# Optimization experiments

Measured on AMD Instinct MI355X. Metric: run time of the kernel, lower is better.

Reference implementation:

```python
import jax, jax.numpy as jnp
import numpy as np
import math

B, S, H, D = 1, 2048, 12, 128
DIM = H * D
BLKQ, BLKK = 128, 64
TOPK = 0.2
EPS = 1e-6
NEG = -1e30


def setup_inputs() -> dict:
    key = jax.random.key(0)
    ks = jax.random.split(key, 8)
    hidden_states = jax.random.normal(ks[0], (B, S, DIM), jnp.float32)
    # interleaved RoPE tables: even slots hold cos, odd slots hold sin phase copies
    pos = np.arange(S, dtype=np.float64)[:, None]
    inv = 1.0 / (10000.0 ** (np.arange(0, D, 2, dtype=np.float64) / D))
    ang = pos * inv[None, :]                       # [S, D/2]
    freqs_cos = jnp.asarray(np.repeat(np.cos(ang), 2, axis=-1), jnp.float32).reshape(1, S, 1, D)
    freqs_sin = jnp.asarray(np.repeat(np.sin(ang), 2, axis=-1), jnp.float32).reshape(1, S, 1, D)
    sc = 1.0 / math.sqrt(DIM)
    Wq = jax.random.normal(ks[1], (DIM, DIM), jnp.float32) * sc
    Wk = jax.random.normal(ks[2], (DIM, DIM), jnp.float32) * sc
    Wv = jax.random.normal(ks[3], (DIM, DIM), jnp.float32) * sc
    Wo = jax.random.normal(ks[4], (DIM, DIM), jnp.float32) * sc
    bq = jax.random.normal(ks[5], (DIM,), jnp.float32) * 0.01
    bk = jax.random.normal(ks[6], (DIM,), jnp.float32) * 0.01
    bv = jax.random.normal(ks[7], (DIM,), jnp.float32) * 0.01
    bo = jnp.zeros((DIM,), jnp.float32)
    gq = jnp.ones((DIM,), jnp.float32)
    gk = jnp.ones((DIM,), jnp.float32)
    return dict(hidden_states=hidden_states, freqs_cos=freqs_cos, freqs_sin=freqs_sin,
                Wq=Wq, bq=bq, Wk=Wk, bk=bk, Wv=Wv, bv=bv, Wo=Wo, bo=bo, gq=gq, gk=gk)


def _rmsnorm(x, g):
    return x * jax.lax.rsqrt(jnp.mean(x * x, axis=-1, keepdims=True) + EPS) * g


def _rope(x, fc, fs):
    # x: [B,S,H,D]; interleaved even/odd rotation as in _apply_rotary_emb
    x1 = x[..., 0::2]
    x2 = x[..., 1::2]
    cos = fc[..., 0::2]
    sin = fs[..., 1::2]
    even = x1 * cos - x2 * sin
    odd = x1 * sin + x2 * cos
    return jnp.stack([even, odd], axis=-1).reshape(x.shape)


def _sla(q, k, v):
    # q,k,v: [B,H,S,D]. Top-k block-sparse exact attention + linear attention
    # (softmax feature map) on the unselected blocks, jointly normalized.
    nqb, nkb = S // BLKQ, S // BLKK
    ksel = max(1, int(math.ceil(TOPK * nkb)))
    qb = q.reshape(B, H, nqb, BLKQ, D).mean(axis=3)
    kb = k.reshape(B, H, nkb, BLKK, D).mean(axis=3)
    blk_scores = jnp.einsum('bhqd,bhkd->bhqk', qb, kb)
    _, idx = jax.lax.top_k(blk_scores, ksel)                  # [B,H,nqb,ksel]
    bmask = (jax.nn.one_hot(idx, nkb, dtype=jnp.float32).sum(axis=-2) > 0)
    mask = jnp.repeat(jnp.repeat(bmask, BLKQ, axis=2), BLKK, axis=3)  # [B,H,S,S]

    scale = 1.0 / math.sqrt(D)
    s = jnp.einsum('bhqd,bhkd->bhqk', q, k) * scale
    m = jnp.max(jnp.where(mask, s, NEG), axis=-1, keepdims=True)
    p = jnp.where(mask, jnp.exp(s - m), 0.0)
    num_s = jnp.einsum('bhqk,bhkd->bhqd', p, v)
    den_s = p.sum(axis=-1, keepdims=True)

    lq = jax.nn.softmax(q, axis=-1)
    lk = jax.nn.softmax(k, axis=-1)
    L = jnp.where(mask, 0.0, jnp.einsum('bhqd,bhkd->bhqk', lq, lk))
    num_l = jnp.einsum('bhqk,bhkd->bhqd', L, v)
    den_l = L.sum(axis=-1, keepdims=True)

    w = jnp.exp(-m)  # bring linear part onto the max-shifted exp scale
    return (num_s + w * num_l) / (den_s + w * den_l)


def reference(hidden_states, freqs_cos, freqs_sin, Wq, bq, Wk, bk, Wv, bv, Wo, bo, gq, gk):
    q = _rmsnorm(hidden_states @ Wq + bq, gq).reshape(B, S, H, D)
    k = _rmsnorm(hidden_states @ Wk + bk, gk).reshape(B, S, H, D)
    v = (hidden_states @ Wv + bv).reshape(B, S, H, D)
    q = _rope(q, freqs_cos, freqs_sin)
    k = _rope(k, freqs_cos, freqs_sin)
    q, k, v = (t.transpose(0, 2, 1, 3) for t in (q, k, v))  # [B,H,S,D]
    o = _sla(q, k, v)
    o = o.transpose(0, 2, 1, 3).reshape(B, S, DIM)
    return o @ Wo + bo
```

## Files before the change

### kernel.cpp

```cpp
#include <hip/hip_runtime.h>
#include <hip/hip_bf16.h>

#define SQ   2048
#define DIMM 1536
#define QS   4608
#define NH   12
#define DH   128
#define NQB  16
#define NKB  32
#define KSEL 7

typedef unsigned short u16;
typedef __bf16 bf16x8 __attribute__((ext_vector_type(8)));
typedef _Float16 f16x8 __attribute__((ext_vector_type(8)));
typedef short  s16x8  __attribute__((ext_vector_type(8)));
typedef float  f32x4  __attribute__((ext_vector_type(4)));

__device__ __forceinline__ float bf2f(u16 u) {
  unsigned int x = ((unsigned int)u) << 16;
  return __builtin_bit_cast(float, x);
}
__device__ __forceinline__ u16 f2bf(float f) {
  unsigned int x = __builtin_bit_cast(unsigned int, f);
  x += 0x7fffu + ((x >> 16) & 1u);
  return (u16)(x >> 16);
}

typedef __attribute__((address_space(3))) void lds_vt;
typedef const __attribute__((address_space(1))) void g_vt;
__device__ __forceinline__ void dma16(const void* g, void* l) {
  __builtin_amdgcn_global_load_lds((g_vt*)g, (lds_vt*)l, 16, 0, 0);
}

__global__ __launch_bounds__(256) void prep_hs(const float* __restrict__ hs,
                                               u16* __restrict__ hh,
                                               u16* __restrict__ hl) {
  size_t i = ((size_t)blockIdx.x * 256 + threadIdx.x) * 8;
  f32x4 a = *(const f32x4*)&hs[i];
  f32x4 b = *(const f32x4*)&hs[i + 4];
  s16x8 h, l;
  #pragma unroll
  for (int j = 0; j < 4; j++) {
    u16 hj = f2bf(a[j]); h[j] = (short)hj; l[j] = (short)f2bf(a[j] - bf2f(hj));
    u16 hk = f2bf(b[j]); h[4 + j] = (short)hk; l[4 + j] = (short)f2bf(b[j] - bf2f(hk));
  }
  *(s16x8*)&hh[i] = h;
  *(s16x8*)&hl[i] = l;
}

__global__ __launch_bounds__(256) void prep_w(const float* __restrict__ W0,
                                              const float* __restrict__ W1,
                                              const float* __restrict__ W2,
                                              const float* __restrict__ W3,
                                              u16* __restrict__ WTh,
                                              u16* __restrict__ WTl) {
  __shared__ float tile[64][65];
  int wi = blockIdx.z;
  const float* W = (wi == 0) ? W0 : (wi == 1) ? W1 : (wi == 2) ? W2 : W3;
  int x = threadIdx.x & 63, y = threadIdx.x >> 6;
  int k0 = blockIdx.y * 64, n0 = blockIdx.x * 64;
  #pragma unroll
  for (int i = 0; i < 16; i++) {
    int k = y + i * 4;
    tile[k][x] = W[(size_t)(k0 + k) * DIMM + n0 + x];
  }
  __syncthreads();
  size_t obase = (size_t)wi * DIMM * DIMM;
  #pragma unroll
  for (int i = 0; i < 16; i++) {
    int n = y + i * 4;
    float v = tile[x][n];
    size_t oi = obase + (size_t)(n0 + n) * DIMM + k0 + x;
    if (wi == 3) {
      WTh[oi] = __builtin_bit_cast(u16, (_Float16)v);
    } else {
      u16 h = f2bf(v);
      WTh[oi] = h;
      WTl[oi] = f2bf(v - bf2f(h));
    }
  }
}

__global__ __launch_bounds__(256) void gemm3_k(const u16* __restrict__ Ahp,
                                               const u16* __restrict__ Alp,
                                               const u16* __restrict__ WTh,
                                               const u16* __restrict__ WTl,
                                               const float* __restrict__ bq,
                                               const float* __restrict__ bk,
                                               const float* __restrict__ bv,
                                               float* __restrict__ C) {
  __shared__ u16 As[2][128][64];
  __shared__ u16 Bs[2][128][64];
  const int tid = threadIdx.x;
  const int w = tid >> 6, lane = tid & 63, quad = lane >> 4, l16 = lane & 15;
  const int wr = w >> 1, wc = w & 1;
  const int m_base = blockIdx.y * 128;
  const int nt = blockIdx.x;
  const int wi = nt / 12;
  const int n_in = (nt % 12) * 128;
  const u16* Bh0 = WTh + ((size_t)wi * DIMM + n_in) * DIMM;
  const u16* Bl0 = WTl + ((size_t)wi * DIMM + n_in) * DIMM;
  const float* bias = (wi == 0) ? bq : (wi == 1) ? bk : bv;
  const bool split = (wi != 2);

  const int srow = lane >> 3;
  const int skc = (((lane & 7) ^ srow) * 8);
  const int rx = (l16 & 7);

  f32x4 zero4 = {0.f, 0.f, 0.f, 0.f};
  f32x4 acc[4][4];
  #pragma unroll
  for (int i = 0; i < 4; i++)
    #pragma unroll
    for (int j = 0; j < 4; j++) acc[i][j] = zero4;

  for (int k0 = 0; k0 < DIMM; k0 += 64) {
    #pragma unroll
    for (int c = 0; c < 4; c++) {
      int r0 = w * 32 + c * 8;
      int row = r0 + srow;
      dma16(&Ahp[(size_t)(m_base + row) * DIMM + k0 + skc], &As[0][r0][0]);
      dma16(&Bh0[(size_t)row * DIMM + k0 + skc], &Bs[0][r0][0]);
      if (split) {
        dma16(&Alp[(size_t)(m_base + row) * DIMM + k0 + skc], &As[1][r0][0]);
        dma16(&Bl0[(size_t)row * DIMM + k0 + skc], &Bs[1][r0][0]);
      }
    }
    __syncthreads();
    #pragma unroll
    for (int kk = 0; kk < 2; kk++) {
      const int coff = ((kk * 4 + quad) ^ rx) * 8;
      bf16x8 afh[4], afl[4], bfh[4], bfl[4];
      #pragma unroll
      for (int i = 0; i < 4; i++)
        afh[i] = __builtin_bit_cast(bf16x8,
                 *(const s16x8*)&As[0][wr * 64 + i * 16 + l16][coff]);
      #pragma unroll
      for (int j = 0; j < 4; j++)
        bfh[j] = __builtin_bit_cast(bf16x8,
                 *(const s16x8*)&Bs[0][wc * 64 + j * 16 + l16][coff]);
      if (split) {
        #pragma unroll
        for (int i = 0; i < 4; i++)
          afl[i] = __builtin_bit_cast(bf16x8,
                   *(const s16x8*)&As[1][wr * 64 + i * 16 + l16][coff]);
        #pragma unroll
        for (int j = 0; j < 4; j++)
          bfl[j] = __builtin_bit_cast(bf16x8,
                   *(const s16x8*)&Bs[1][wc * 64 + j * 16 + l16][coff]);
      }
      #pragma unroll
      for (int i = 0; i < 4; i++)
        #pragma unroll
        for (int j = 0; j < 4; j++) {
          acc[i][j] = __builtin_amdgcn_mfma_f32_16x16x32_bf16(afh[i], bfh[j], acc[i][j], 0, 0, 0);
          if (split) {
            acc[i][j] = __builtin_amdgcn_mfma_f32_16x16x32_bf16(afh[i], bfl[j], acc[i][j], 0, 0, 0);
            acc[i][j] = __builtin_amdgcn_mfma_f32_16x16x32_bf16(afl[i], bfh[j], acc[i][j], 0, 0, 0);
          }
        }
    }
    __syncthreads();
  }
  #pragma unroll
  for (int i = 0; i < 4; i++)
    #pragma unroll
    for (int j = 0; j < 4; j++) {
      int tc = wc * 64 + j * 16 + l16;
      float bv2 = bias[n_in + tc];
      #pragma unroll
      for (int rg = 0; rg < 4; rg++) {
        int r = m_base + wr * 64 + i * 16 + quad * 4 + rg;
        C[(size_t)r * QS + nt * 128 + tc] = acc[i][j][rg] + bv2;
      }
    }
}

__global__ __launch_bounds__(256) void gemm_o(const u16* __restrict__ Ap,
                                              const u16* __restrict__ Bp,
                                              const float* __restrict__ bias,
                                              float* __restrict__ C) {
  __shared__ u16 As[64][64];
  __shared__ u16 Bs[128][64];
  const int tid = threadIdx.x;
  const int w = tid >> 6, lane = tid & 63, quad = lane >> 4, l16 = lane & 15;
  const int wr = w >> 1, wc = w & 1;
  const int m_base = blockIdx.y * 64, n_base = blockIdx.x * 128;
  const int srow = lane >> 3;
  const int skc = (((lane & 7) ^ srow) * 8);
  const int rx = (l16 & 7);

  f32x4 zero4 = {0.f, 0.f, 0.f, 0.f};
  f32x4 acc[2][4];
  #pragma unroll
  for (int i = 0; i < 2; i++)
    #pragma unroll
    for (int j = 0; j < 4; j++) acc[i][j] = zero4;

  for (int k0 = 0; k0 < DIMM; k0 += 64) {
    #pragma unroll
    for (int c = 0; c < 2; c++) {
      int r0 = w * 16 + c * 8;
      int row = r0 + srow;
      dma16(&Ap[(size_t)(m_base + row) * DIMM + k0 + skc], &As[r0][0]);
    }
    #pragma unroll
    for (int c = 0; c < 4; c++) {
      int r0 = w * 32 + c * 8;
      int row = r0 + srow;
      dma16(&Bp[(size_t)(n_base + row) * DIMM + k0 + skc], &Bs[r0][0]);
    }
    __syncthreads();
    #pragma unroll
    for (int kk = 0; kk < 2; kk++) {
      const int coff = ((kk * 4 + quad) ^ rx) * 8;
      f16x8 af[2], bf[4];
      #pragma unroll
      for (int i = 0; i < 2; i++)
        af[i] = __builtin_bit_cast(f16x8,
                *(const s16x8*)&As[wr * 32 + i * 16 + l16][coff]);
      #pragma unroll
      for (int j = 0; j < 4; j++)
        bf[j] = __builtin_bit_cast(f16x8,
                *(const s16x8*)&Bs[wc * 64 + j * 16 + l16][coff]);
      #pragma unroll
      for (int i = 0; i < 2; i++)
        #pragma unroll
        for (int j = 0; j < 4; j++)
          acc[i][j] = __builtin_amdgcn_mfma_f32_16x16x32_f16(af[i], bf[j], acc[i][j], 0, 0, 0);
    }
    __syncthreads();
  }
  #pragma unroll
  for (int i = 0; i < 2; i++)
    #pragma unroll
    for (int j = 0; j < 4; j++) {
      int c = n_base + wc * 64 + j * 16 + l16;
      float bv2 = bias[c];
      #pragma unroll
      for (int rg = 0; rg < 4; rg++) {
        int r = m_base + wr * 32 + i * 16 + quad * 4 + rg;
        C[(size_t)r * DIMM + c] = acc[i][j][rg] + bv2;
      }
    }
}

__global__ __launch_bounds__(256) void norm_rope_k(float* __restrict__ qkv,
                                                   const float* __restrict__ gq,
                                                   const float* __restrict__ gk,
                                                   const float* __restrict__ fc,
                                                   const float* __restrict__ fs) {
  int s = blockIdx.x;
  float* row = qkv + (size_t)s * QS + (blockIdx.y == 0 ? 0 : DIMM);
  const float* g = (blockIdx.y == 0) ? gq : gk;
  int t = threadIdx.x;
  float ss = 0.f;
  #pragma unroll
  for (int i = 0; i < 6; i++) {
    float v = row[t + i * 256];
    ss += v * v;
  }
  #pragma unroll
  for (int m = 1; m < 64; m <<= 1) ss += __shfl_xor(ss, m, 64);
  __shared__ float wsum[4];
  if ((t & 63) == 0) wsum[t >> 6] = ss;
  __syncthreads();
  float tot = wsum[0] + wsum[1] + wsum[2] + wsum[3];
  float sc = rsqrtf(tot / 1536.0f + 1e-6f);
  #pragma unroll
  for (int i = 0; i < 3; i++) {
    int p = t + i * 256;
    int h = p >> 6, ip = p & 63;
    int base = h * 128 + 2 * ip;
    float x1 = row[base] * sc * g[base];
    float x2 = row[base + 1] * sc * g[base + 1];
    float c = fc[(size_t)s * 128 + 2 * ip];
    float sn = fs[(size_t)s * 128 + 2 * ip + 1];
    row[base]     = x1 * c - x2 * sn;
    row[base + 1] = x1 * sn + x2 * c;
  }
}

__global__ __launch_bounds__(256) void prep_qk(const float* __restrict__ qkv,
                                               u16* __restrict__ qbf,
                                               u16* __restrict__ kbf) {
  int s0 = blockIdx.x * 128, h = blockIdx.y, z = blockIdx.z;
  int off = z * DIMM;
  u16* out = (z ? kbf : qbf) + ((size_t)h * SQ + s0) * 128;
  int tid = threadIdx.x;
  #pragma unroll
  for (int i = 0; i < 8; i++) {
    int idx = i * 256 + tid;
    int r = idx >> 4, c = idx & 15;
    int g = (c & 8) | ((c ^ (r & 7)) & 7);
    const float* src = qkv + (size_t)(s0 + r) * QS + off + h * DH + g * 8;
    f32x4 a = *(const f32x4*)src;
    f32x4 b = *(const f32x4*)(src + 4);
    s16x8 o;
    #pragma unroll
    for (int e = 0; e < 4; e++) { o[e] = (short)f2bf(a[e]); o[4 + e] = (short)f2bf(b[e]); }
    *(s16x8*)&out[r * 128 + c * 8] = o;
  }
}

__global__ __launch_bounds__(256) void prep_vT(const float* __restrict__ vf,
                                               u16* __restrict__ vbfT) {
  __shared__ float vt[64][132];
  int b = blockIdx.x, h = blockIdx.y, tid = threadIdx.x;
  #pragma unroll
  for (int i = 0; i < 8; i++) {
    int idx = i * 256 + tid; int key = idx >> 5, d4 = (idx & 31) * 4;
    *(f32x4*)&vt[key][d4] = *(const f32x4*)&vf[(size_t)(b * 64 + key) * QS + h * DH + d4];
  }
  __syncthreads();
  u16* out = vbfT + ((size_t)(h * NKB + b)) * 128 * 64;
  #pragma unroll
  for (int i = 0; i < 4; i++) {
    int idx = i * 256 + tid;
    int d = idx >> 3, c = idx & 7;
    int g = c ^ (d & 7);
    s16x8 o;
    #pragma unroll
    for (int e = 0; e < 8; e++) o[e] = (short)f2bf(vt[g * 8 + e][d]);
    *(s16x8*)&out[d * 64 + c * 8] = o;
  }
}

__global__ __launch_bounds__(128) void means_k(const float* __restrict__ qf,
                                               const float* __restrict__ kf,
                                               float* __restrict__ qb,
                                               float* __restrict__ kb) {
  int h = blockIdx.y, t = threadIdx.x;
  if (blockIdx.x < NQB) {
    int qi = blockIdx.x;
    float a = 0.f;
    for (int r = 0; r < 128; r++) a += qf[(size_t)(qi * 128 + r) * QS + h * DH + t];
    qb[(h * NQB + qi) * DH + t] = a * (1.0f / 128.0f);
  } else {
    int ki = blockIdx.x - NQB;
    float a = 0.f;
    for (int r = 0; r < 64; r++) a += kf[(size_t)(ki * 64 + r) * QS + h * DH + t];
    kb[(h * NKB + ki) * DH + t] = a * (1.0f / 64.0f);
  }
}

__global__ __launch_bounds__(64) void topk_k(const float* __restrict__ qb,
                                             const float* __restrict__ kb,
                                             int* __restrict__ sel) {
  int h = blockIdx.y, qi = blockIdx.x, t = threadIdx.x;
  __shared__ float scs[NKB];
  if (t < NKB) {
    float a = 0.f;
    for (int d = 0; d < DH; d++)
      a += qb[(h * NQB + qi) * DH + d] * kb[(h * NKB + t) * DH + d];
    scs[t] = a;
  }
  __syncthreads();
  if (t == 0) {
    unsigned int used = 0;
    for (int it = 0; it < KSEL; it++) {
      float best = -3.4e38f; int bi = 0;
      for (int j = 0; j < NKB; j++)
        if (!((used >> j) & 1) && scs[j] > best) { best = scs[j]; bi = j; }
      used |= 1u << bi;
      sel[(h * NQB + qi) * 8 + it] = bi;
    }
  }
}

__global__ __launch_bounds__(256) void kv_k(const float* __restrict__ kf,
                                            const float* __restrict__ vf,
                                            float* __restrict__ KV,
                                            float* __restrict__ slk) {
  int h = blockIdx.y, kb = blockIdx.x, t = threadIdx.x;
  __shared__ float lkt[64][128];
  __shared__ float vt[64][128];
  #pragma unroll
  for (int i = 0; i < 8; i++) {
    int idx = i * 256 + t; int r = idx >> 5, d4 = (idx & 31) * 4;
    *(f32x4*)&vt[r][d4] = *(const f32x4*)&vf[(size_t)(kb * 64 + r) * QS + h * DH + d4];
  }
  if (t < 64) {
    const float* kr = kf + (size_t)(kb * 64 + t) * QS + h * DH;
    float m = -3.4e38f;
    for (int d = 0; d < 128; d++) m = fmaxf(m, kr[d]);
    float sum = 0.f;
    for (int d = 0; d < 128; d++) { float e = __expf(kr[d] - m); lkt[t][d] = e; sum += e; }
    float inv = 1.0f / sum;
    for (int d = 0; d < 128; d++) lkt[t][d] *= inv;
  }
  __syncthreads();
  int d1 = t >> 1, hf = t & 1;
  float acc[64];
  #pragma unroll
  for (int i = 0; i < 64; i++) acc[i] = 0.f;
  for (int j = 0; j < 64; j++) {
    float lv = lkt[j][d1];
    #pragma unroll
    for (int dd = 0; dd < 64; dd++) acc[dd] += lv * vt[j][hf * 64 + dd];
  }
  float* out = KV + ((size_t)(h * NKB + kb) * DH + d1) * DH + hf * 64;
  #pragma unroll
  for (int dd = 0; dd < 64; dd++) out[dd] = acc[dd];
  if (t < 128) {
    float a = 0.f;
    for (int j = 0; j < 64; j++) a += lkt[j][t];
    slk[(h * NKB + kb) * DH + t] = a;
  }
}

__global__ __launch_bounds__(256) void kvtot_k(const float* __restrict__ KV,
                                               const float* __restrict__ slk,
                                               float* __restrict__ KVtot,
                                               float* __restrict__ sltot) {
  int h = blockIdx.y; int e = blockIdx.x * 256 + threadIdx.x;
  float a = 0.f;
  for (int b = 0; b < NKB; b++) a += KV[(size_t)(h * NKB + b) * 16384 + e];
  KVtot[(size_t)h * 16384 + e] = a;
  if (blockIdx.x == 0 && threadIdx.x < 128) {
    float s2 = 0.f;
    for (int b = 0; b < NKB; b++) s2 += slk[(h * NKB + b) * DH + threadIdx.x];
    sltot[h * DH + threadIdx.x] = s2;
  }
}

__global__ __launch_bounds__(256) void attn_k(const u16* __restrict__ qbf,
                                              const u16* __restrict__ kbf,
                                              const u16* __restrict__ vbfT,
                                              const int* __restrict__ sel,
                                              const float* __restrict__ KV,
                                              const float* __restrict__ slk,
                                              const float* __restrict__ KVtot,
                                              const float* __restrict__ sltot,
                                              u16* __restrict__ of16) {
  __shared__ u16 qt[128 * 128];
  __shared__ u16 kt[64 * 128];
  __shared__ u16 vtT[128 * 64];
  __shared__ u16 ptb[128][72];
  __shared__ u16 MT[128][136];
  __shared__ float mrow[128], lrow[128], dent[128], slsh[128];
  __shared__ int selsh[KSEL];

  int h = blockIdx.y, qi = blockIdx.x, tid = threadIdx.x;
  int w = tid >> 6, lane = tid & 63, quad = lane >> 4, l16 = lane & 15;

  {
    const u16* qsrc = qbf + ((size_t)h * SQ + qi * 128) * 128;
    #pragma unroll
    for (int c = 0; c < 8; c++)
      dma16(qsrc + (w * 32 + c * 4) * 128 + lane * 8, &qt[(w * 32 + c * 4) * 128]);
  }
  if (tid < KSEL) selsh[tid] = sel[(h * NQB + qi) * 8 + tid];
  __syncthreads();

  float m_run[2][4], l_run[2][4];
  f32x4 zero4 = {0.f, 0.f, 0.f, 0.f};
  f32x4 oacc[2][8];
  #pragma unroll
  for (int mt = 0; mt < 2; mt++) {
    #pragma unroll
    for (int rg = 0; rg < 4; rg++) { m_run[mt][rg] = -3.0e38f; l_run[mt][rg] = 0.f; }
    #pragma unroll
    for (int nt = 0; nt < 8; nt++) oacc[mt][nt] = zero4;
  }

  for (int bi = 0; bi < KSEL; bi++) {
    int b = selsh[bi];
    {
      const u16* ksrc = kbf + ((size_t)h * SQ + b * 64) * 128;
      #pragma unroll
      for (int c = 0; c < 4; c++)
        dma16(ksrc + (w * 16 + c * 4) * 128 + lane * 8, &kt[(w * 16 + c * 4) * 128]);
      const u16* vsrc = vbfT + ((size_t)(h * NKB + b)) * 128 * 64;
      #pragma unroll
      for (int c = 0; c < 4; c++)
        dma16(vsrc + (w * 32 + c * 8) * 64 + lane * 8, &vtT[(w * 32 + c * 8) * 64]);
    }
    __syncthreads();

    f32x4 sacc[2][4];
    #pragma unroll
    for (int mt = 0; mt < 2; mt++)
      #pragma unroll
      for (int nt = 0; nt < 4; nt++) sacc[mt][nt] = zero4;
    #pragma unroll
    for (int kk = 0; kk < 4; kk++) {
      const int kkq = kk * 4 + quad;
      const int qoff = ((kkq & 8) | ((kkq ^ (l16 & 7)) & 7)) * 8;
      bf16x8 af[2], bfr[4];
      af[0] = __builtin_bit_cast(bf16x8, *(const s16x8*)&qt[(w * 32 + l16) * 128 + qoff]);
      af[1] = __builtin_bit_cast(bf16x8, *(const s16x8*)&qt[(w * 32 + 16 + l16) * 128 + qoff]);
      #pragma unroll
      for (int nt = 0; nt < 4; nt++)
        bfr[nt] = __builtin_bit_cast(bf16x8, *(const s16x8*)&kt[(nt * 16 + l16) * 128 + qoff]);
      #pragma unroll
      for (int mt = 0; mt < 2; mt++)
        #pragma unroll
        for (int nt = 0; nt < 4; nt++)
          sacc[mt][nt] = __builtin_amdgcn_mfma_f32_16x16x32_bf16(af[mt], bfr[nt], sacc[mt][nt], 0, 0, 0);
    }
    const float SCALE = 0.08838834764831845f;
    #pragma unroll
    for (int mt = 0; mt < 2; mt++)
      #pragma unroll
      for (int nt = 0; nt < 4; nt++) sacc[mt][nt] *= SCALE;

    #pragma unroll
    for (int mt = 0; mt < 2; mt++) {
      #pragma unroll
      for (int rg = 0; rg < 4; rg++) {
        float bmax = fmaxf(fmaxf(sacc[mt][0][rg], sacc[mt][1][rg]),
                           fmaxf(sacc[mt][2][rg], sacc[mt][3][rg]));
        bmax = fmaxf(bmax, __shfl_xor(bmax, 1, 64));
        bmax = fmaxf(bmax, __shfl_xor(bmax, 2, 64));
        bmax = fmaxf(bmax, __shfl_xor(bmax, 4, 64));
        bmax = fmaxf(bmax, __shfl_xor(bmax, 8, 64));
        float mold = m_run[mt][rg];
        float mnew = fmaxf(mold, bmax);
        float alpha = __expf(mold - mnew);
        float rs = 0.f;
        #pragma unroll
        for (int nt = 0; nt < 4; nt++) {
          float p = __expf(sacc[mt][nt][rg] - mnew);
          sacc[mt][nt][rg] = p; rs += p;
        }
        rs += __shfl_xor(rs, 1, 64);
        rs += __shfl_xor(rs, 2, 64);
        rs += __shfl_xor(rs, 4, 64);
        rs += __shfl_xor(rs, 8, 64);
        m_run[mt][rg] = mnew;
        l_run[mt][rg] = l_run[mt][rg] * alpha + rs;
        #pragma unroll
        for (int nt = 0; nt < 8; nt++) oacc[mt][nt][rg] *= alpha;
        int r = w * 32 + mt * 16 + quad * 4 + rg;
        #pragma unroll
        for (int nt = 0; nt < 4; nt++) ptb[r][nt * 16 + l16] = f2bf(sacc[mt][nt][rg]);
      }
    }
    __syncthreads();
    #pragma unroll
    for (int kk = 0; kk < 2; kk++) {
      bf16x8 pa[2];
      pa[0] = __builtin_bit_cast(bf16x8, *(const s16x8*)&ptb[w * 32 + l16][kk * 32 + quad * 8]);
      pa[1] = __builtin_bit_cast(bf16x8, *(const s16x8*)&ptb[w * 32 + 16 + l16][kk * 32 + quad * 8]);
      #pragma unroll
      for (int nt = 0; nt < 8; nt++) {
        const int voff = ((kk * 4 + quad) ^ (l16 & 7)) * 8;
        bf16x8 vb = __builtin_bit_cast(bf16x8, *(const s16x8*)&vtT[(nt * 16 + l16) * 64 + voff]);
        oacc[0][nt] = __builtin_amdgcn_mfma_f32_16x16x32_bf16(pa[0], vb, oacc[0][nt], 0, 0, 0);
        oacc[1][nt] = __builtin_amdgcn_mfma_f32_16x16x32_bf16(pa[1], vb, oacc[1][nt], 0, 0, 0);
      }
    }
    __syncthreads();
  }

  if (l16 == 0) {
    #pragma unroll
    for (int mt = 0; mt < 2; mt++)
      #pragma unroll
      for (int rg = 0; rg < 4; rg++) {
        int r = w * 32 + mt * 16 + quad * 4 + rg;
        mrow[r] = m_run[mt][rg];
        lrow[r] = l_run[mt][rg];
      }
  }
  if (tid < 128) {
    float a = sltot[h * DH + tid];
    #pragma unroll
    for (int i = 0; i < KSEL; i++) a -= slk[(h * NKB + selsh[i]) * DH + tid];
    slsh[tid] = a;
  }
  for (int i = 0; i < 16; i++) {
    int idx = i * 256 + tid;
    int e4 = idx * 4;
    int d1 = e4 >> 7, d2 = e4 & 127;
    f32x4 a = *(const f32x4*)&KVtot[(size_t)h * 16384 + e4];
    #pragma unroll
    for (int k2 = 0; k2 < KSEL; k2++) {
      f32x4 s4 = *(const f32x4*)&KV[(size_t)(h * NKB + selsh[k2]) * 16384 + e4];
      a -= s4;
    }
    #pragma unroll
    for (int j = 0; j < 4; j++) MT[d2 + j][d1] = f2bf(a[j]);
  }
  __syncthreads();

  {
    int r = tid >> 1, hf2 = tid & 1;
    float w_r = __expf(-mrow[r]);
    float mx = -3.4e38f;
    #pragma unroll
    for (int g = 0; g < 8; g++) {
      int gc = hf2 * 8 + g;
      int c = (gc & 8) | ((gc ^ (r & 7)) & 7);
      #pragma unroll
      for (int e = 0; e < 8; e++) mx = fmaxf(mx, bf2f(qt[r * 128 + c * 8 + e]));
    }
    mx = fmaxf(mx, __shfl_xor(mx, 1, 64));
    float sum = 0.f;
    #pragma unroll
    for (int g = 0; g < 8; g++) {
      int gc = hf2 * 8 + g;
      int c = (gc & 8) | ((gc ^ (r & 7)) & 7);
      #pragma unroll
      for (int e = 0; e < 8; e++) sum += __expf(bf2f(qt[r * 128 + c * 8 + e]) - mx);
    }
    sum += __shfl_xor(sum, 1, 64);
    float sc2 = w_r / sum;
    float dl = 0.f;
    #pragma unroll
    for (int g = 0; g < 8; g++) {
      int gc = hf2 * 8 + g;
      int c = (gc & 8) | ((gc ^ (r & 7)) & 7);
      #pragma unroll
      for (int e = 0; e < 8; e++) {
        float lq = __expf(bf2f(qt[r * 128 + c * 8 + e]) - mx) * sc2;
        dl += lq * slsh[gc * 8 + e];
        qt[r * 128 + c * 8 + e] = f2bf(lq);
      }
    }
    dl += __shfl_xor(dl, 1, 64);
    if (hf2 == 0) dent[r] = lrow[r] + dl;
  }
  __syncthreads();

  #pragma unroll
  for (int kk = 0; kk < 4; kk++) {
    const int kkq = kk * 4 + quad;
    const int qoff = ((kkq & 8) | ((kkq ^ (l16 & 7)) & 7)) * 8;
    bf16x8 af0 = __builtin_bit_cast(bf16x8, *(const s16x8*)&qt[(w * 32 + l16) * 128 + qoff]);
    bf16x8 af1 = __builtin_bit_cast(bf16x8, *(const s16x8*)&qt[(w * 32 + 16 + l16) * 128 + qoff]);
    #pragma unroll
    for (int nt = 0; nt < 8; nt++) {
      bf16x8 mb = __builtin_bit_cast(bf16x8, *(const s16x8*)&MT[nt * 16 + l16][kk * 32 + quad * 8]);
      oacc[0][nt] = __builtin_amdgcn_mfma_f32_16x16x32_bf16(af0, mb, oacc[0][nt], 0, 0, 0);
      oacc[1][nt] = __builtin_amdgcn_mfma_f32_16x16x32_bf16(af1, mb, oacc[1][nt], 0, 0, 0);
    }
  }

  #pragma unroll
  for (int mt = 0; mt < 2; mt++)
    #pragma unroll
    for (int rg = 0; rg < 4; rg++) {
      int r = w * 32 + mt * 16 + quad * 4 + rg;
      float inv = 1.0f / dent[r];
      #pragma unroll
      for (int nt = 0; nt < 8; nt++) {
        int c = nt * 16 + l16;
        float v = oacc[mt][nt][rg] * inv;
        size_t oi = (size_t)(qi * 128 + r) * DIMM + h * DH + c;
        of16[oi] = __builtin_bit_cast(u16, (_Float16)v);
      }
    }
}

extern "C" void kernel_launch(void* const* d_in, const int* in_sizes, int n_in,
                              void* d_out, int out_size, void* d_ws, size_t ws_size,
                              hipStream_t stream) {
  const float* hs = (const float*)d_in[0];
  const float* fc = (const float*)d_in[1];
  const float* fs = (const float*)d_in[2];
  const float* Wq = (const float*)d_in[3];
  const float* bq = (const float*)d_in[4];
  const float* Wk = (const float*)d_in[5];
  const float* bk = (const float*)d_in[6];
  const float* Wv = (const float*)d_in[7];
  const float* bv = (const float*)d_in[8];
  const float* Wo = (const float*)d_in[9];
  const float* bo = (const float*)d_in[10];
  const float* gq = (const float*)d_in[11];
  const float* gk = (const float*)d_in[12];

  char* p = (char*)d_ws;
  auto alloc = [&](size_t bytes) {
    char* r = p; p += (bytes + 255) & ~(size_t)255; return r;
  };
  u16* WTh = (u16*)alloc((size_t)4 * DIMM * DIMM * 2);
  u16* WTl = (u16*)alloc((size_t)4 * DIMM * DIMM * 2);
  u16* hsh = (u16*)alloc((size_t)SQ * DIMM * 2);
  u16* hsl = (u16*)alloc((size_t)SQ * DIMM * 2);
  float* qkv = (float*)alloc((size_t)SQ * QS * 4);
  u16* qbf = (u16*)alloc((size_t)NH * SQ * DH * 2);
  u16* kbf = (u16*)alloc((size_t)NH * SQ * DH * 2);
  u16* vbfT = (u16*)alloc((size_t)NH * NKB * DH * 64 * 2);
  float* qb = (float*)alloc((size_t)NH * NQB * DH * 4);
  float* kb = (float*)alloc((size_t)NH * NKB * DH * 4);
  int* sel = (int*)alloc((size_t)NH * NQB * 8 * 4);
  float* KV = (float*)alloc((size_t)NH * NKB * DH * DH * 4);
  float* slk = (float*)alloc((size_t)NH * NKB * DH * 4);
  float* KVtot = (float*)alloc((size_t)NH * DH * DH * 4);
  float* sltot = (float*)alloc((size_t)NH * DH * 4);

  float* qf = qkv;
  float* kf = qkv + DIMM;
  float* vf = qkv + 2 * DIMM;

  prep_hs<<<SQ * DIMM / (256 * 8), 256, 0, stream>>>(hs, hsh, hsl);
  prep_w<<<dim3(24, 24, 4), 256, 0, stream>>>(Wq, Wk, Wv, Wo, WTh, WTl);

  gemm3_k<<<dim3(36, 16), 256, 0, stream>>>(hsh, hsl, WTh, WTl, bq, bk, bv, qkv);

  norm_rope_k<<<dim3(SQ, 2), 256, 0, stream>>>(qkv, gq, gk, fc, fs);
  means_k<<<dim3(NQB + NKB, NH), 128, 0, stream>>>(qf, kf, qb, kb);
  topk_k<<<dim3(NQB, NH), 64, 0, stream>>>(qb, kb, sel);
  kv_k<<<dim3(NKB, NH), 256, 0, stream>>>(kf, vf, KV, slk);
  kvtot_k<<<dim3(64, NH), 256, 0, stream>>>(KV, slk, KVtot, sltot);
  prep_qk<<<dim3(16, NH, 2), 256, 0, stream>>>(qkv, qbf, kbf);
  prep_vT<<<dim3(NKB, NH), 256, 0, stream>>>(vf, vbfT);

  u16* of16 = hsh;
  attn_k<<<dim3(NQB, NH), 256, 0, stream>>>(qbf, kbf, vbfT, sel, KV, slk, KVtot, sltot, of16);

  const u16* WTo = WTh + (size_t)3 * DIMM * DIMM;
  gemm_o<<<dim3(12, 32), 256, 0, stream>>>(of16, WTo, bo, (float*)d_out);
}
```

Baseline: 369.0 us.

## Fuse bf16 Q/K packing into norm-rope, split attention blocks, vectorize kv_k

Several independent changes. The norm/RoPE kernel now also writes the swizzled bf16 Q/K copies directly, so the separate prep_qk pass and its reread of qkv go away. The attention kernel handles 64 query rows per block instead of 128, doubling the grid to 384 blocks for better CU occupancy. It also aliases shared-memory buffers to cut LDS use and raises wave priority around the MFMA sections. kv_k now computes the key softmax with all 256 threads and vectorized loads, pads its LDS rows, and accumulates with float4 vectors; in exchange the attention block's K/V loads are spread over twice as many blocks.

```diff
diff --git a/kernel.cpp b/kernel.cpp
--- a/kernel.cpp
+++ b/kernel.cpp
@@ -249,10 +249,13 @@
                                                    const float* __restrict__ gq,
                                                    const float* __restrict__ gk,
                                                    const float* __restrict__ fc,
-                                                   const float* __restrict__ fs) {
+                                                   const float* __restrict__ fs,
+                                                   u16* __restrict__ qbf,
+                                                   u16* __restrict__ kbf) {
   int s = blockIdx.x;
   float* row = qkv + (size_t)s * QS + (blockIdx.y == 0 ? 0 : DIMM);
   const float* g = (blockIdx.y == 0) ? gq : gk;
+  u16* obase = (blockIdx.y == 0) ? qbf : kbf;
   int t = threadIdx.x;
   float ss = 0.f;
   #pragma unroll
@@ -276,30 +279,15 @@
     float x2 = row[base + 1] * sc * g[base + 1];
     float c = fc[(size_t)s * 128 + 2 * ip];
     float sn = fs[(size_t)s * 128 + 2 * ip + 1];
-    row[base]     = x1 * c - x2 * sn;
-    row[base + 1] = x1 * sn + x2 * c;
-  }
-}
-
-__global__ __launch_bounds__(256) void prep_qk(const float* __restrict__ qkv,
-                                               u16* __restrict__ qbf,
-                                               u16* __restrict__ kbf) {
-  int s0 = blockIdx.x * 128, h = blockIdx.y, z = blockIdx.z;
-  int off = z * DIMM;
-  u16* out = (z ? kbf : qbf) + ((size_t)h * SQ + s0) * 128;
-  int tid = threadIdx.x;
-  #pragma unroll
-  for (int i = 0; i < 8; i++) {
-    int idx = i * 256 + tid;
-    int r = idx >> 4, c = idx & 15;
-    int g = (c & 8) | ((c ^ (r & 7)) & 7);
-    const float* src = qkv + (size_t)(s0 + r) * QS + off + h * DH + g * 8;
-    f32x4 a = *(const f32x4*)src;
-    f32x4 b = *(const f32x4*)(src + 4);
-    s16x8 o;
-    #pragma unroll
-    for (int e = 0; e < 4; e++) { o[e] = (short)f2bf(a[e]); o[4 + e] = (short)f2bf(b[e]); }
-    *(s16x8*)&out[r * 128 + c * 8] = o;
+    float ev = x1 * c - x2 * sn;
+    float od = x1 * sn + x2 * c;
+    row[base]     = ev;
+    row[base + 1] = od;
+    int gsk = ip >> 2, e = (2 * ip) & 7;
+    int cc = (gsk & 8) | ((gsk ^ (s & 7)) & 7);
+    u16* ob = obase + ((size_t)h * SQ + s) * 128;
+    unsigned int pack = (unsigned int)f2bf(ev) | ((unsigned int)f2bf(od) << 16);
+    *(unsigned int*)&ob[cc * 8 + e] = pack;
   }
 }
 
@@ -373,39 +361,61 @@
                                             float* __restrict__ KV,
                                             float* __restrict__ slk) {
   int h = blockIdx.y, kb = blockIdx.x, t = threadIdx.x;
-  __shared__ float lkt[64][128];
-  __shared__ float vt[64][128];
+  __shared__ float lkt[64][132];
+  __shared__ float vt[64][132];
   #pragma unroll
   for (int i = 0; i < 8; i++) {
     int idx = i * 256 + t; int r = idx >> 5, d4 = (idx & 31) * 4;
     *(f32x4*)&vt[r][d4] = *(const f32x4*)&vf[(size_t)(kb * 64 + r) * QS + h * DH + d4];
   }
-  if (t < 64) {
-    const float* kr = kf + (size_t)(kb * 64 + t) * QS + h * DH;
-    float m = -3.4e38f;
-    for (int d = 0; d < 128; d++) m = fmaxf(m, kr[d]);
+  {
+    int r = t >> 2, q4 = t & 3;
+    const float* kr = kf + (size_t)(kb * 64 + r) * QS + h * DH;
+    f32x4 x[8];
+    float mx = -3.4e38f;
+    #pragma unroll
+    for (int i = 0; i < 8; i++) {
+      x[i] = *(const f32x4*)&kr[q4 * 32 + i * 4];
+      mx = fmaxf(mx, fmaxf(fmaxf(x[i][0], x[i][1]), fmaxf(x[i][2], x[i][3])));
+    }
+    mx = fmaxf(mx, __shfl_xor(mx, 1, 64));
+    mx = fmaxf(mx, __shfl_xor(mx, 2, 64));
     float sum = 0.f;
-    for (int d = 0; d < 128; d++) { float e = __expf(kr[d] - m); lkt[t][d] = e; sum += e; }
+    #pragma unroll
+    for (int i = 0; i < 8; i++) {
+      #pragma unroll
+      for (int e = 0; e < 4; e++) { float v = __expf(x[i][e] - mx); x[i][e] = v; sum += v; }
+    }
+    sum += __shfl_xor(sum, 1, 64);
+    sum += __shfl_xor(sum, 2, 64);
     float inv = 1.0f / sum;
-    for (int d = 0; d < 128; d++) lkt[t][d] *= inv;
+    #pragma unroll
+    for (int i = 0; i < 8; i++) {
+      x[i] *= inv;
+      *(f32x4*)&lkt[r][q4 * 32 + i * 4] = x[i];
+    }
   }
   __syncthreads();
   int d1 = t >> 1, hf = t & 1;
-  float acc[64];
-  #pragma unroll
-  for (int i = 0; i < 64; i++) acc[i] = 0.f;
+  f32x4 a[16];
+  f32x4 zero4 = {0.f, 0.f, 0.f, 0.f};
+  #pragma unroll
+  for (int i = 0; i < 16; i++) a[i] = zero4;
   for (int j = 0; j < 64; j++) {
     float lv = lkt[j][d1];
     #pragma unroll
-    for (int dd = 0; dd < 64; dd++) acc[dd] += lv * vt[j][hf * 64 + dd];
+    for (int q = 0; q < 16; q++) {
+      f32x4 vv = *(const f32x4*)&vt[j][hf * 64 + q * 4];
+      a[q] += lv * vv;
+    }
   }
   float* out = KV + ((size_t)(h * NKB + kb) * DH + d1) * DH + hf * 64;
   #pragma unroll
-  for (int dd = 0; dd < 64; dd++) out[dd] = acc[dd];
+  for (int q = 0; q < 16; q++) *(f32x4*)&out[q * 4] = a[q];
   if (t < 128) {
-    float a = 0.f;
-    for (int j = 0; j < 64; j++) a += lkt[j][t];
-    slk[(h * NKB + kb) * DH + t] = a;
+    float s2 = 0.f;
+    for (int j = 0; j < 64; j++) s2 += lkt[j][t];
+    slk[(h * NKB + kb) * DH + t] = s2;
   }
 }
 
@@ -433,36 +443,34 @@
                                               const float* __restrict__ KVtot,
                                               const float* __restrict__ sltot,
                                               u16* __restrict__ of16) {
-  __shared__ u16 qt[128 * 128];
-  __shared__ u16 kt[64 * 128];
-  __shared__ u16 vtT[128 * 64];
-  __shared__ u16 ptb[128][72];
-  __shared__ u16 MT[128][136];
-  __shared__ float mrow[128], lrow[128], dent[128], slsh[128];
+  __shared__ u16 smem[25600];
+  __shared__ float mrow[64], lrow[64], dent[64], slsh[128];
   __shared__ int selsh[KSEL];
+  u16* qt  = smem;
+  u16* vtT = smem + 8192;
+  u16* kt  = smem + 16384;
+  u16* ptb = smem + 16384;
+  u16* MT  = smem + 8192;
 
   int h = blockIdx.y, qi = blockIdx.x, tid = threadIdx.x;
   int w = tid >> 6, lane = tid & 63, quad = lane >> 4, l16 = lane & 15;
 
   {
-    const u16* qsrc = qbf + ((size_t)h * SQ + qi * 128) * 128;
-    #pragma unroll
-    for (int c = 0; c < 8; c++)
-      dma16(qsrc + (w * 32 + c * 4) * 128 + lane * 8, &qt[(w * 32 + c * 4) * 128]);
-  }
-  if (tid < KSEL) selsh[tid] = sel[(h * NQB + qi) * 8 + tid];
+    const u16* qsrc = qbf + ((size_t)h * SQ + qi * 64) * 128;
+    #pragma unroll
+    for (int c = 0; c < 4; c++)
+      dma16(qsrc + (w * 16 + c * 4) * 128 + lane * 8, &qt[(w * 16 + c * 4) * 128]);
+  }
+  if (tid < KSEL) selsh[tid] = sel[(h * NQB + (qi >> 1)) * 8 + tid];
   __syncthreads();
 
-  float m_run[2][4], l_run[2][4];
+  float m_run[4], l_run[4];
   f32x4 zero4 = {0.f, 0.f, 0.f, 0.f};
-  f32x4 oacc[2][8];
-  #pragma unroll
-  for (int mt = 0; mt < 2; mt++) {
-    #pragma unroll
-    for (int rg = 0; rg < 4; rg++) { m_run[mt][rg] = -3.0e38f; l_run[mt][rg] = 0.f; }
-    #pragma unroll
-    for (int nt = 0; nt < 8; nt++) oacc[mt][nt] = zero4;
-  }
+  f32x4 oacc[8];
+  #pragma unroll
+  for (int rg = 0; rg < 4; rg++) { m_run[rg] = -3.0e38f; l_run[rg] = 0.f; }
+  #pragma unroll
+  for (int nt = 0; nt < 8; nt++) oacc[nt] = zero4;
 
   for (int bi = 0; bi < KSEL; bi++) {
     int b = selsh[bi];
@@ -478,91 +486,83 @@
     }
     __syncthreads();
 
-    f32x4 sacc[2][4];
-    #pragma unroll
-    for (int mt = 0; mt < 2; mt++)
-      #pragma unroll
-      for (int nt = 0; nt < 4; nt++) sacc[mt][nt] = zero4;
+    f32x4 sacc[4];
+    #pragma unroll
+    for (int nt = 0; nt < 4; nt++) sacc[nt] = zero4;
+    __builtin_amdgcn_s_setprio(1);
     #pragma unroll
     for (int kk = 0; kk < 4; kk++) {
       const int kkq = kk * 4 + quad;
       const int qoff = ((kkq & 8) | ((kkq ^ (l16 & 7)) & 7)) * 8;
-      bf16x8 af[2], bfr[4];
-      af[0] = __builtin_bit_cast(bf16x8, *(const s16x8*)&qt[(w * 32 + l16) * 128 + qoff]);
-      af[1] = __builtin_bit_cast(bf16x8, *(const s16x8*)&qt[(w * 32 + 16 + l16) * 128 + qoff]);
-      #pragma unroll
-      for (int nt = 0; nt < 4; nt++)
-        bfr[nt] = __builtin_bit_cast(bf16x8, *(const s16x8*)&kt[(nt * 16 + l16) * 128 + qoff]);
-      #pragma unroll
-      for (int mt = 0; mt < 2; mt++)
-        #pragma unroll
-        for (int nt = 0; nt < 4; nt++)
-          sacc[mt][nt] = __builtin_amdgcn_mfma_f32_16x16x32_bf16(af[mt], bfr[nt], sacc[mt][nt], 0, 0, 0);
-    }
+      bf16x8 af = __builtin_bit_cast(bf16x8, *(const s16x8*)&qt[(w * 16 + l16) * 128 + qoff]);
+      #pragma unroll
+      for (int nt = 0; nt < 4; nt++) {
+        bf16x8 bfr = __builtin_bit_cast(bf16x8, *(const s16x8*)&kt[(nt * 16 + l16) * 128 + qoff]);
+        sacc[nt] = __builtin_amdgcn_mfma_f32_16x16x32_bf16(af, bfr, sacc[nt], 0, 0, 0);
+      }
+    }
+    __builtin_amdgcn_s_setprio(0);
     const float SCALE = 0.08838834764831845f;
     #pragma unroll
-    for (int mt = 0; mt < 2; mt++)
-      #pragma unroll
-      for (int nt = 0; nt < 4; nt++) sacc[mt][nt] *= SCALE;
-
-    #pragma unroll
-    for (int mt = 0; mt < 2; mt++) {
-      #pragma unroll
-      for (int rg = 0; rg < 4; rg++) {
-        float bmax = fmaxf(fmaxf(sacc[mt][0][rg], sacc[mt][1][rg]),
-                           fmaxf(sacc[mt][2][rg], sacc[mt][3][rg]));
-        bmax = fmaxf(bmax, __shfl_xor(bmax, 1, 64));
-        bmax = fmaxf(bmax, __shfl_xor(bmax, 2, 64));
-        bmax = fmaxf(bmax, __shfl_xor(bmax, 4, 64));
-        bmax = fmaxf(bmax, __shfl_xor(bmax, 8, 64));
-        float mold = m_run[mt][rg];
-        float mnew = fmaxf(mold, bmax);
-        float alpha = __expf(mold - mnew);
-        float rs = 0.f;
-        #pragma unroll
-        for (int nt = 0; nt < 4; nt++) {
-          float p = __expf(sacc[mt][nt][rg] - mnew);
-          sacc[mt][nt][rg] = p; rs += p;
-        }
-        rs += __shfl_xor(rs, 1, 64);
-        rs += __shfl_xor(rs, 2, 64);
-        rs += __shfl_xor(rs, 4, 64);
-        rs += __shfl_xor(rs, 8, 64);
-        m_run[mt][rg] = mnew;
-        l_run[mt][rg] = l_run[mt][rg] * alpha + rs;
-        #pragma unroll
-        for (int nt = 0; nt < 8; nt++) oacc[mt][nt][rg] *= alpha;
-        int r = w * 32 + mt * 16 + quad * 4 + rg;
-        #pragma unroll
-        for (int nt = 0; nt < 4; nt++) ptb[r][nt * 16 + l16] = f2bf(sacc[mt][nt][rg]);
+    for (int nt = 0; nt < 4; nt++) sacc[nt] *= SCALE;
+
+    #pragma unroll
+    for (int rg = 0; rg < 4; rg++) {
+      float bmax = fmaxf(fmaxf(sacc[0][rg], sacc[1][rg]),
+                         fmaxf(sacc[2][rg], sacc[3][rg]));
+      bmax = fmaxf(bmax, __shfl_xor(bmax, 1, 64));
+      bmax = fmaxf(bmax, __shfl_xor(bmax, 2, 64));
+      bmax = fmaxf(bmax, __shfl_xor(bmax, 4, 64));
+      bmax = fmaxf(bmax, __shfl_xor(bmax, 8, 64));
+      float mold = m_run[rg];
+      float mnew = fmaxf(mold, bmax);
+      float alpha = __expf(mold - mnew);
+      float rs = 0.f;
+      #pragma unroll
+      for (int nt = 0; nt < 4; nt++) {
+        float p = __expf(sacc[nt][rg] - mnew);
+        sacc[nt][rg] = p; rs += p;
       }
+      rs += __shfl_xor(rs, 1, 64);
+      rs += __shfl_xor(rs, 2, 64);
+      rs += __shfl_xor(rs, 4, 64);
+      rs += __shfl_xor(rs, 8, 64);
+      m_run[rg] = mnew;
+      l_run[rg] = l_run[rg] * alpha + rs;
+      #pragma unroll
+      for (int nt = 0; nt < 8; nt++) oacc[nt][rg] *= alpha;
     }
     __syncthreads();
     #pragma unroll
+    for (int rg = 0; rg < 4; rg++) {
+      int r = w * 16 + quad * 4 + rg;
+      #pragma unroll
+      for (int nt = 0; nt < 4; nt++) ptb[r * 72 + nt * 16 + l16] = f2bf(sacc[nt][rg]);
+    }
+    __syncthreads();
+
+    __builtin_amdgcn_s_setprio(1);
+    #pragma unroll
     for (int kk = 0; kk < 2; kk++) {
-      bf16x8 pa[2];
-      pa[0] = __builtin_bit_cast(bf16x8, *(const s16x8*)&ptb[w * 32 + l16][kk * 32 + quad * 8]);
-      pa[1] = __builtin_bit_cast(bf16x8, *(const s16x8*)&ptb[w * 32 + 16 + l16][kk * 32 + quad * 8]);
+      bf16x8 pa = __builtin_bit_cast(bf16x8, *(const s16x8*)&ptb[(w * 16 + l16) * 72 + kk * 32 + quad * 8]);
       #pragma unroll
       for (int nt = 0; nt < 8; nt++) {
         const int voff = ((kk * 4 + quad) ^ (l16 & 7)) * 8;
         bf16x8 vb = __builtin_bit_cast(bf16x8, *(const s16x8*)&vtT[(nt * 16 + l16) * 64 + voff]);
-        oacc[0][nt] = __builtin_amdgcn_mfma_f32_16x16x32_bf16(pa[0], vb, oacc[0][nt], 0, 0, 0);
-        oacc[1][nt] = __builtin_amdgcn_mfma_f32_16x16x32_bf16(pa[1], vb, oacc[1][nt], 0, 0, 0);
+        oacc[nt] = __builtin_amdgcn_mfma_f32_16x16x32_bf16(pa, vb, oacc[nt], 0, 0, 0);
       }
     }
+    __builtin_amdgcn_s_setprio(0);
     __syncthreads();
   }
 
   if (l16 == 0) {
     #pragma unroll
-    for (int mt = 0; mt < 2; mt++)
-      #pragma unroll
-      for (int rg = 0; rg < 4; rg++) {
-        int r = w * 32 + mt * 16 + quad * 4 + rg;
-        mrow[r] = m_run[mt][rg];
-        lrow[r] = l_run[mt][rg];
-      }
+    for (int rg = 0; rg < 4; rg++) {
+      int r = w * 16 + quad * 4 + rg;
+      mrow[r] = m_run[rg];
+      lrow[r] = l_run[rg];
+    }
   }
   if (tid < 128) {
     float a = sltot[h * DH + tid];
@@ -581,36 +581,38 @@
       a -= s4;
     }
     #pragma unroll
-    for (int j = 0; j < 4; j++) MT[d2 + j][d1] = f2bf(a[j]);
+    for (int j = 0; j < 4; j++) MT[(d2 + j) * 136 + d1] = f2bf(a[j]);
   }
   __syncthreads();
 
   {
-    int r = tid >> 1, hf2 = tid & 1;
+    int r = tid >> 2, sub = tid & 3;
     float w_r = __expf(-mrow[r]);
     float mx = -3.4e38f;
     #pragma unroll
-    for (int g = 0; g < 8; g++) {
-      int gc = hf2 * 8 + g;
+    for (int gi = 0; gi < 4; gi++) {
+      int gc = sub * 4 + gi;
       int c = (gc & 8) | ((gc ^ (r & 7)) & 7);
       #pragma unroll
       for (int e = 0; e < 8; e++) mx = fmaxf(mx, bf2f(qt[r * 128 + c * 8 + e]));
     }
     mx = fmaxf(mx, __shfl_xor(mx, 1, 64));
+    mx = fmaxf(mx, __shfl_xor(mx, 2, 64));
     float sum = 0.f;
     #pragma unroll
-    for (int g = 0; g < 8; g++) {
-      int gc = hf2 * 8 + g;
+    for (int gi = 0; gi < 4; gi++) {
+      int gc = sub * 4 + gi;
       int c = (gc & 8) | ((gc ^ (r & 7)) & 7);
       #pragma unroll
       for (int e = 0; e < 8; e++) sum += __expf(bf2f(qt[r * 128 + c * 8 + e]) - mx);
     }
     sum += __shfl_xor(sum, 1, 64);
+    sum += __shfl_xor(sum, 2, 64);
     float sc2 = w_r / sum;
     float dl = 0.f;
     #pragma unroll
-    for (int g = 0; g < 8; g++) {
-      int gc = hf2 * 8 + g;
+    for (int gi = 0; gi < 4; gi++) {
+      int gc = sub * 4 + gi;
       int c = (gc & 8) | ((gc ^ (r & 7)) & 7);
       #pragma unroll
       for (int e = 0; e < 8; e++) {
@@ -620,38 +622,37 @@
       }
     }
     dl += __shfl_xor(dl, 1, 64);
-    if (hf2 == 0) dent[r] = lrow[r] + dl;
+    dl += __shfl_xor(dl, 2, 64);
+    if (sub == 0) dent[r] = lrow[r] + dl;
   }
   __syncthreads();
 
+  __builtin_amdgcn_s_setprio(1);
   #pragma unroll
   for (int kk = 0; kk < 4; kk++) {
     const int kkq = kk * 4 + quad;
     const int qoff = ((kkq & 8) | ((kkq ^ (l16 & 7)) & 7)) * 8;
-    bf16x8 af0 = __builtin_bit_cast(bf16x8, *(const s16x8*)&qt[(w * 32 + l16) * 128 + qoff]);
-    bf16x8 af1 = __builtin_bit_cast(bf16x8, *(const s16x8*)&qt[(w * 32 + 16 + l16) * 128 + qoff]);
+    bf16x8 af = __builtin_bit_cast(bf16x8, *(const s16x8*)&qt[(w * 16 + l16) * 128 + qoff]);
     #pragma unroll
     for (int nt = 0; nt < 8; nt++) {
-      bf16x8 mb = __builtin_bit_cast(bf16x8, *(const s16x8*)&MT[nt * 16 + l16][kk * 32 + quad * 8]);
-      oacc[0][nt] = __builtin_amdgcn_mfma_f32_16x16x32_bf16(af0, mb, oacc[0][nt], 0, 0, 0);
-      oacc[1][nt] = __builtin_amdgcn_mfma_f32_16x16x32_bf16(af1, mb, oacc[1][nt], 0, 0, 0);
-    }
-  }
-
-  #pragma unroll
-  for (int mt = 0; mt < 2; mt++)
-    #pragma unroll
-    for (int rg = 0; rg < 4; rg++) {
-      int r = w * 32 + mt * 16 + quad * 4 + rg;
-      float inv = 1.0f / dent[r];
-      #pragma unroll
-      for (int nt = 0; nt < 8; nt++) {
-        int c = nt * 16 + l16;
-        float v = oacc[mt][nt][rg] * inv;
-        size_t oi = (size_t)(qi * 128 + r) * DIMM + h * DH + c;
-        of16[oi] = __builtin_bit_cast(u16, (_Float16)v);
-      }
-    }
+      bf16x8 mb = __builtin_bit_cast(bf16x8, *(const s16x8*)&MT[(nt * 16 + l16) * 136 + kk * 32 + quad * 8]);
+      oacc[nt] = __builtin_amdgcn_mfma_f32_16x16x32_bf16(af, mb, oacc[nt], 0, 0, 0);
+    }
+  }
+  __builtin_amdgcn_s_setprio(0);
+
+  #pragma unroll
+  for (int rg = 0; rg < 4; rg++) {
+    int r = w * 16 + quad * 4 + rg;
+    float inv = 1.0f / dent[r];
+    #pragma unroll
+    for (int nt = 0; nt < 8; nt++) {
+      int c = nt * 16 + l16;
+      float v = oacc[nt][rg] * inv;
+      size_t oi = (size_t)(qi * 64 + r) * DIMM + h * DH + c;
+      of16[oi] = __builtin_bit_cast(u16, (_Float16)v);
+    }
+  }
 }
 
 extern "C" void kernel_launch(void* const* d_in, const int* in_sizes, int n_in,
@@ -700,16 +701,15 @@
 
   gemm3_k<<<dim3(36, 16), 256, 0, stream>>>(hsh, hsl, WTh, WTl, bq, bk, bv, qkv);
 
-  norm_rope_k<<<dim3(SQ, 2), 256, 0, stream>>>(qkv, gq, gk, fc, fs);
+  norm_rope_k<<<dim3(SQ, 2), 256, 0, stream>>>(qkv, gq, gk, fc, fs, qbf, kbf);
   means_k<<<dim3(NQB + NKB, NH), 128, 0, stream>>>(qf, kf, qb, kb);
   topk_k<<<dim3(NQB, NH), 64, 0, stream>>>(qb, kb, sel);
   kv_k<<<dim3(NKB, NH), 256, 0, stream>>>(kf, vf, KV, slk);
   kvtot_k<<<dim3(64, NH), 256, 0, stream>>>(KV, slk, KVtot, sltot);
-  prep_qk<<<dim3(16, NH, 2), 256, 0, stream>>>(qkv, qbf, kbf);
   prep_vT<<<dim3(NKB, NH), 256, 0, stream>>>(vf, vbfT);
 
   u16* of16 = hsh;
-  attn_k<<<dim3(NQB, NH), 256, 0, stream>>>(qbf, kbf, vbfT, sel, KV, slk, KVtot, sltot, of16);
+  attn_k<<<dim3(2 * NQB, NH), 256, 0, stream>>>(qbf, kbf, vbfT, sel, KV, slk, KVtot, sltot, of16);
 
   const u16* WTo = WTh + (size_t)3 * DIMM * DIMM;
   gemm_o<<<dim3(12, 32), 256, 0, stream>>>(of16, WTo, bo, (float*)d_out);
```

Result: faster. 349.8 us (-5.2%).
